# Kernel optimization log

Hardware: AMD Instinct MI355X
Metric: run time of the kernel (lower is better)

## Reference

```python
import jax, jax.numpy as jnp
import numpy as np

IMG = 256      # image size implied by 8x8 grid * scale 32
THRE = 0.5
DIS = 4        # img_dislocate_size
B = 64


def _shift_map(s, size, dis):
    # Pixel-level coordinate map for the dislocated half: cell r starts at
    # max(r*s - dis, 0) (the torch while-loop clamps negative coords to 0).
    p = jnp.arange(size)
    base = jnp.maximum((p // s) * s - dis, 0)
    return base + p % s


def _cell_norm(x, g, s):
    # Per-cell (crop) min/max normalization, matching the per-crop
    # (t - min) / (max - min + 1e-5) in HeatMaptoImg.
    b = x.shape[0]
    v = x.reshape(b, 1, g, s, g, s)
    mn = v.min(axis=(3, 5), keepdims=True)
    mx = v.max(axis=(3, 5), keepdims=True)
    return ((v - mn) / (mx - mn + 1e-5)).reshape(b, 1, g * s, g * s)


def setup_inputs() -> dict:
    key = jax.random.key(0)
    ks = jax.random.split(key, 7)
    B2 = 2 * B
    return {
        "img": jax.random.uniform(ks[0], (B, 1, IMG, IMG), jnp.float32),
        "heat8": jax.random.uniform(ks[1], (B2, 1, 8, 8), jnp.float32),
        "heat16": jax.random.uniform(ks[2], (B2, 1, 16, 16), jnp.float32),
        "heat32": jax.random.uniform(ks[3], (B2, 1, 32, 32), jnp.float32),
        "seg8": jax.random.uniform(ks[4], (B2, 1, IMG, IMG), jnp.float32),
        "seg16": jax.random.uniform(ks[5], (B2, 1, IMG, IMG), jnp.float32),
        "seg32": jax.random.uniform(ks[6], (B2, 1, IMG, IMG), jnp.float32),
    }


def reference(img, heat8, heat16, heat32, seg8, seg16, seg32):
    Bv = img.shape[0]
    label = jnp.zeros((Bv, 1, IMG, IMG), img.dtype)
    cnt = jnp.zeros_like(label)
    crops = {}
    # fine grid (scale 8) processed first, matching the reversed loop order
    for heat, seg, g in ((heat32, seg32, 32), (heat16, seg16, 16), (heat8, seg8, 8)):
        s = IMG // g                      # crop / cell size for this scale
        mask = (heat > THRE).astype(img.dtype)          # (2B,1,g,g)
        mask_pix = jnp.repeat(jnp.repeat(mask, s, axis=2), s, axis=3)  # (2B,1,256,256)
        Y = _shift_map(s, IMG, DIS)
        # dislocated half crops come from the shifted image region
        img_d = img[:, :, Y[:, None], Y[None, :]]       # (B,1,256,256)
        both = jnp.concatenate([img, img_d], axis=0)    # (2B,1,256,256)
        crops[g] = _cell_norm(both, g, s) * mask_pix
        # UnitLabels: scatter-add per-crop labels + counts, then average
        ca = mask_pix[:Bv]
        label = label + ca * seg[:Bv]
        cnt = cnt + ca
        cd = mask_pix[Bv:]
        label = label.at[:, :, Y[:, None], Y[None, :]].add(cd * seg[Bv:])
        cnt = cnt.at[:, :, Y[:, None], Y[None, :]].add(cd)
    label = label / (cnt + 1e-10)
    return (crops[32], crops[16], crops[8], label)
```

## Files before the change

kernel.cpp:

```cpp
#include <hip/hip_runtime.h>

#define IMG   256
#define IMG2  65536
#define NB    64
#define NB2   128


#define WS_A8   0
#define WS_B8   65536
#define WS_A16  131072
#define WS_B16  147456
#define WS_A32  163840
#define WS_B32  167936

template <int S, int G>
__device__ __forceinline__ void cell_stats(
    const float* __restrict__ img, const float* __restrict__ heat,
    float2* __restrict__ ws, int idx, int half, int wsbase) {
    const int b  = idx / (G * G);
    const int rr = idx % (G * G);
    const int ci = rr / G;
    const int cj = rr % G;
    const int r0 = half ? max(ci * S - 4, 0) : ci * S;
    const int c0 = half ? max(cj * S - 4, 0) : cj * S;
    const float* __restrict__ p = img + (size_t)b * IMG2 + r0 * IMG + c0;
    float mn = 3.4e38f, mx = -3.4e38f;
    for (int r = 0; r < S; ++r) {
#pragma unroll
        for (int c = 0; c < S; c += 4) {
            const float4 q = *(const float4*)(p + r * IMG + c);
            mn = fminf(mn, fminf(fminf(q.x, q.y), fminf(q.z, q.w)));
            mx = fmaxf(mx, fmaxf(fmaxf(q.x, q.y), fmaxf(q.z, q.w)));
        }
    }
    const float h   = heat[(size_t)(b + half * NB) * (G * G) + ci * G + cj];
    const float inv = (h > 0.5f ? 1.0f : 0.0f) / (mx - mn + 1e-5f);
    ws[wsbase + idx] = make_float2(mn, inv);
}

__global__ __launch_bounds__(256) void stats_kernel(
    const float* __restrict__ img,
    const float* __restrict__ heat8,
    const float* __restrict__ heat16,
    const float* __restrict__ heat32,
    float2* __restrict__ ws) {
    const int t = blockIdx.x * 256 + threadIdx.x;
    if (t < 131072) {
        const int half = t >> 16;
        cell_stats<8, 32>(img, heat32, ws, t & 65535, half,
                          half ? WS_B8 : WS_A8);
    } else if (t < 163840) {
        const int tt = t - 131072;
        const int half = tt >> 14;
        cell_stats<16, 16>(img, heat16, ws, tt & 16383, half,
                           half ? WS_B16 : WS_A16);
    } else {
        const int tt = t - 163840;
        const int half = tt >> 12;
        cell_stats<32, 8>(img, heat8, ws, tt & 4095, half,
                          half ? WS_B32 : WS_A32);
    }
}

__device__ __forceinline__ float4 nrm(float4 q, float2 st) {
    float4 o;
    o.x = (q.x - st.x) * st.y; o.y = (q.y - st.x) * st.y;
    o.z = (q.z - st.x) * st.y; o.w = (q.w - st.x) * st.y;
    return o;
}

__global__ __launch_bounds__(256) void crops_stream_kernel(
    const float* __restrict__ img,
    const float2* __restrict__ ws,
    float* __restrict__ out) {
    const int w    = threadIdx.x >> 6;
    const int lane = threadIdx.x & 63;
    const int lid  = blockIdx.x * 4 + w;
    const int b    = lid >> 8;
    const int u    = lid & 255;
    const int v0   = lane << 2;
    const int vm   = max(v0 - 4, 0);

    const float* __restrict__ ip = img + (size_t)b * IMG2;

    const int u8  = ((u >> 3) ? (u & ~7)  - 4 : 0) + (u & 7);
    const int u16 = ((u >> 4) ? (u & ~15) - 4 : 0) + (u & 15);
    const int u32 = ((u >> 5) ? (u & ~31) - 4 : 0) + (u & 31);

    const float4 xa  = *(const float4*)(ip + u   * IMG + v0);
    const float4 q08 = *(const float4*)(ip + u8  * IMG + v0);
    const float4 qm8 = *(const float4*)(ip + u8  * IMG + vm);
    const float4 q16 = *(const float4*)(ip + u16 * IMG + v0);
    const float4 qm6 = *(const float4*)(ip + u16 * IMG + vm);
    const float4 q32 = *(const float4*)(ip + u32 * IMG + v0);
    const float4 qm2 = *(const float4*)(ip + u32 * IMG + vm);

    const float2 a8  = ws[WS_A8  + ((b << 5) + (u >> 3)) * 32 + (v0 >> 3)];
    const float2 b8  = ws[WS_B8  + ((b << 5) + (u >> 3)) * 32 + (v0 >> 3)];
    const float2 a16 = ws[WS_A16 + ((b << 4) + (u >> 4)) * 16 + (v0 >> 4)];
    const float2 b16 = ws[WS_B16 + ((b << 4) + (u >> 4)) * 16 + (v0 >> 4)];
    const float2 a32 = ws[WS_A32 + ((b << 3) + (u >> 5)) *  8 + (v0 >> 5)];
    const float2 b32 = ws[WS_B32 + ((b << 3) + (u >> 5)) *  8 + (v0 >> 5)];

    const float4 s8v = (v0 < 8)  ? q08 : qm8;
    const float4 s16v = (v0 < 16) ? q16 : qm6;
    const float4 s32v = (v0 < 32) ? q32 : qm2;

    const size_t rowA = (size_t)b * IMG2 + u * IMG + v0;
    const size_t rowB = (size_t)(b + NB) * IMG2 + u * IMG + v0;
    float* __restrict__ c32 = out;
    float* __restrict__ c16 = out + (size_t)NB2 * IMG2;
    float* __restrict__ c8  = out + (size_t)2 * NB2 * IMG2;

    *(float4*)(c32 + rowA) = nrm(xa,  a8);
    *(float4*)(c32 + rowB) = nrm(s8v, b8);
    *(float4*)(c16 + rowA) = nrm(xa,  a16);
    *(float4*)(c16 + rowB) = nrm(s16v, b16);
    *(float4*)(c8  + rowA) = nrm(xa,  a32);
    *(float4*)(c8  + rowB) = nrm(s32v, b32);
}

__device__ __forceinline__ void label_rows(
    const float* __restrict__ heat8,
    const float* __restrict__ heat16,
    const float* __restrict__ heat32,
    const float* __restrict__ seg8,
    const float* __restrict__ seg16,
    const float* __restrict__ seg32,
    float* __restrict__ out,
    int b, int u0) {
    const int wave = threadIdx.x >> 6;
    const int lane = threadIdx.x & 63;
    const int u    = u0 + wave;
    const int v0   = lane << 2;
    const int vs   = min(v0 + 4, 252);

    float nu[4] = {0.f, 0.f, 0.f, 0.f};
    float de[4] = {0.f, 0.f, 0.f, 0.f};

    if (u0 >= 32 && u0 <= 248) {
        const int i1 = u + 4;
#define SCALE_F(heat, seg, g, l, s)                                           \
        {                                                                     \
            const float* __restrict__ h1 = heat + b * (g * g);                \
            const float* __restrict__ h2 = heat + (NB + b) * (g * g);         \
            const float* __restrict__ r1 = seg + (size_t)b * IMG2 + u * IMG;  \
            const float* __restrict__ r2 =                                    \
                seg + (size_t)(NB + b) * IMG2 + i1 * IMG;                     \
            const float4 sd  = *(const float4*)(r1 + v0);                     \
            const float4 sg0 = *(const float4*)(r2 + v0);                     \
            const float4 sg1 = *(const float4*)(r2 + vs);                     \
            const float hd  = h1[(u >> l) * g + (v0 >> l)];                   \
            const float hg0 = h2[(i1 >> l) * g + (v0 >> l)];                  \
            const float hg1 = h2[(i1 >> l) * g + (vs >> l)];                  \
            const float md = (hd > 0.5f) ? 1.0f : 0.0f;                       \
            const float g0 = (hg0 > 0.5f) ? 1.0f : 0.0f;                      \
            const float g1 = (hg1 > 0.5f) ? 1.0f : 0.0f;                      \
            _Pragma("unroll")                                                 \
            for (int c = 0; c < 4; ++c) {                                     \
                const int v = v0 + c;                                         \
                const float m0 = (v < (s)) ? g0 : 0.0f;                       \
                const float m1 = (v >= (s) - 4 && v <= 251) ? g1 : 0.0f;      \
                float x = ((const float*)&sd)[c] * md;                        \
                x = fmaf(m0, ((const float*)&sg0)[c], x);                     \
                x = fmaf(m1, ((const float*)&sg1)[c], x);                     \
                nu[c] += x;                                                   \
                de[c] += md + m0 + m1;                                        \
            }                                                                 \
        }
        SCALE_F(heat32, seg32, 32, 3, 8)
        SCALE_F(heat16, seg16, 16, 4, 16)
        SCALE_F(heat8,  seg8,  8,  5, 32)
#undef SCALE_F
    } else {
        const int i0  = u;
        const int i1c = min(u + 4, 255);
#define SCALE_G(heat, seg, g, l, s)                                           \
        {                                                                     \
            const float* __restrict__ h1 = heat + b * (g * g);                \
            const float* __restrict__ h2 = heat + (NB + b) * (g * g);         \
            const float* __restrict__ r1 = seg + (size_t)b * IMG2 + u * IMG;  \
            const float* __restrict__ ra =                                    \
                seg + (size_t)(NB + b) * IMG2 + i0 * IMG;                     \
            const float* __restrict__ rb =                                    \
                seg + (size_t)(NB + b) * IMG2 + i1c * IMG;                    \
            const float4 sd  = *(const float4*)(r1 + v0);                     \
            const float4 a0q = *(const float4*)(ra + v0);                     \
            const float4 a1q = *(const float4*)(ra + vs);                     \
            const float4 b0q = *(const float4*)(rb + v0);                     \
            const float4 b1q = *(const float4*)(rb + vs);                     \
            const float hd  = h1[(u >> l) * g + (v0 >> l)];                   \
            const float hA0 = h2[(i0 >> l) * g + (v0 >> l)];                  \
            const float hA1 = h2[(i0 >> l) * g + (vs >> l)];                  \
            const float hB0 = h2[(i1c >> l) * g + (v0 >> l)];                 \
            const float hB1 = h2[(i1c >> l) * g + (vs >> l)];                 \
            const float miA = (u < (s)) ? 1.0f : 0.0f;                        \
            const float miB = (u >= (s) - 4 && u <= 251) ? 1.0f : 0.0f;       \
            const float md  = (hd > 0.5f) ? 1.0f : 0.0f;                      \
            const float gA0 = miA * ((hA0 > 0.5f) ? 1.0f : 0.0f);             \
            const float gA1 = miA * ((hA1 > 0.5f) ? 1.0f : 0.0f);             \
            const float gB0 = miB * ((hB0 > 0.5f) ? 1.0f : 0.0f);             \
            const float gB1 = miB * ((hB1 > 0.5f) ? 1.0f : 0.0f);             \
            _Pragma("unroll")                                                 \
            for (int c = 0; c < 4; ++c) {                                     \
                const int v = v0 + c;                                         \
                const float mj0 = (v < (s)) ? 1.0f : 0.0f;                    \
                const float mj1 = (v >= (s) - 4 && v <= 251) ? 1.0f : 0.0f;   \
                const float w00 = gA0 * mj0, w01 = gA1 * mj1;                 \
                const float w10 = gB0 * mj0, w11 = gB1 * mj1;                 \
                float x = ((const float*)&sd)[c] * md;                        \
                x = fmaf(w00, ((const float*)&a0q)[c], x);                    \
                x = fmaf(w01, ((const float*)&a1q)[c], x);                    \
                x = fmaf(w10, ((const float*)&b0q)[c], x);                    \
                x = fmaf(w11, ((const float*)&b1q)[c], x);                    \
                nu[c] += x;                                                   \
                de[c] += md + w00 + w01 + w10 + w11;                          \
            }                                                                 \
        }
        SCALE_G(heat32, seg32, 32, 3, 8)
        SCALE_G(heat16, seg16, 16, 4, 16)
        SCALE_G(heat8,  seg8,  8,  5, 32)
#undef SCALE_G
    }

    float4 o;
    o.x = nu[0] / (de[0] + 1e-10f);
    o.y = nu[1] / (de[1] + 1e-10f);
    o.z = nu[2] / (de[2] + 1e-10f);
    o.w = nu[3] / (de[3] + 1e-10f);
    *(float4*)(out + (size_t)b * IMG2 + u * IMG + v0) = o;
}

__global__ __launch_bounds__(256) void label_kernel(
    const float* __restrict__ heat8,
    const float* __restrict__ heat16,
    const float* __restrict__ heat32,
    const float* __restrict__ seg8,
    const float* __restrict__ seg16,
    const float* __restrict__ seg32,
    float* __restrict__ out) {
    float* label = out + (size_t)3 * NB2 * IMG2;
    const int t  = blockIdx.x;
    label_rows(heat8, heat16, heat32, seg8, seg16, seg32, label,
               t >> 6, (t & 63) << 2);
}

extern "C" void kernel_launch(void* const* d_in, const int* in_sizes, int n_in,
                              void* d_out, int out_size, void* d_ws, size_t ws_size,
                              hipStream_t stream) {
    const float* img    = (const float*)d_in[0];
    const float* heat8  = (const float*)d_in[1];
    const float* heat16 = (const float*)d_in[2];
    const float* heat32 = (const float*)d_in[3];
    const float* seg8   = (const float*)d_in[4];
    const float* seg16  = (const float*)d_in[5];
    const float* seg32  = (const float*)d_in[6];

    stats_kernel<<<dim3(672), 256, 0, stream>>>(
        img, heat8, heat16, heat32, (float2*)d_ws);
    crops_stream_kernel<<<dim3(4096), 256, 0, stream>>>(
        img, (const float2*)d_ws, (float*)d_out);
    label_kernel<<<dim3(4096), 256, 0, stream>>>(
        heat8, heat16, heat32, seg8, seg16, seg32, (float*)d_out);
}
```

Measured before the change: 250.3 us.

## Build cell min/max hierarchically from 4x4 block stats and split crop writes by phase

Adds a pass computing min/max of every 4x4 pixel block, then derives each cell's min/max for all three scales (including the shifted half, which aligns to 4-pixel boundaries) by combining those block stats instead of rescanning the image per cell. The crops kernel is split into six phases across a 6x larger grid, so each thread does one load and one store rather than seven loads and six stores. This removes redundant image reads in the stats stage and cuts per-thread register pressure, at the cost of an extra kernel launch and a workspace round trip.

```diff
diff --git a/kernel.cpp b/kernel.cpp
--- a/kernel.cpp
+++ b/kernel.cpp
@@ -4,7 +4,6 @@
 #define IMG2  65536
 #define NB    64
 #define NB2   128
-
 
 #define WS_A8   0
 #define WS_B8   65536
@@ -12,112 +11,147 @@
 #define WS_B16  147456
 #define WS_A32  163840
 #define WS_B32  167936
-
-template <int S, int G>
-__device__ __forceinline__ void cell_stats(
-    const float* __restrict__ img, const float* __restrict__ heat,
-    float2* __restrict__ ws, int idx, int half, int wsbase) {
-    const int b  = idx / (G * G);
-    const int rr = idx % (G * G);
-    const int ci = rr / G;
-    const int cj = rr % G;
-    const int r0 = half ? max(ci * S - 4, 0) : ci * S;
-    const int c0 = half ? max(cj * S - 4, 0) : cj * S;
-    const float* __restrict__ p = img + (size_t)b * IMG2 + r0 * IMG + c0;
+#define WS_BLK  172032
+
+__global__ __launch_bounds__(256) void blk_kernel(
+    const float* __restrict__ img, float2* __restrict__ ws) {
+    const int wid  = blockIdx.x * 4 + (threadIdx.x >> 6);
+    const int lane = threadIdx.x & 63;
+    const int b    = wid >> 6;
+    const int r4   = wid & 63;
+    const float* __restrict__ p =
+        img + (size_t)b * IMG2 + (r4 * 4) * IMG + lane * 4;
+    const float4 q0 = *(const float4*)(p);
+    const float4 q1 = *(const float4*)(p + IMG);
+    const float4 q2 = *(const float4*)(p + 2 * IMG);
+    const float4 q3 = *(const float4*)(p + 3 * IMG);
+    const float mn01 = fminf(fminf(fminf(q0.x, q0.y), fminf(q0.z, q0.w)),
+                             fminf(fminf(q1.x, q1.y), fminf(q1.z, q1.w)));
+    const float mn23 = fminf(fminf(fminf(q2.x, q2.y), fminf(q2.z, q2.w)),
+                             fminf(fminf(q3.x, q3.y), fminf(q3.z, q3.w)));
+    const float mx01 = fmaxf(fmaxf(fmaxf(q0.x, q0.y), fmaxf(q0.z, q0.w)),
+                             fmaxf(fmaxf(q1.x, q1.y), fmaxf(q1.z, q1.w)));
+    const float mx23 = fmaxf(fmaxf(fmaxf(q2.x, q2.y), fmaxf(q2.z, q2.w)),
+                             fmaxf(fmaxf(q3.x, q3.y), fmaxf(q3.z, q3.w)));
+    ws[WS_BLK + (b << 12) + (r4 << 6) + lane] =
+        make_float2(fminf(mn01, mn23), fmaxf(mx01, mx23));
+}
+
+template <int SH>
+__device__ __forceinline__ float2 combine_blk(
+    const float2* __restrict__ blk, int b, int p0, int q0) {
     float mn = 3.4e38f, mx = -3.4e38f;
-    for (int r = 0; r < S; ++r) {
+    for (int i = 0; i < SH; ++i) {
 #pragma unroll
-        for (int c = 0; c < S; c += 4) {
-            const float4 q = *(const float4*)(p + r * IMG + c);
-            mn = fminf(mn, fminf(fminf(q.x, q.y), fminf(q.z, q.w)));
-            mx = fmaxf(mx, fmaxf(fmaxf(q.x, q.y), fmaxf(q.z, q.w)));
+        for (int j = 0; j < SH; ++j) {
+            const float2 v = blk[(b << 12) + ((p0 + i) << 6) + (q0 + j)];
+            mn = fminf(mn, v.x);
+            mx = fmaxf(mx, v.y);
         }
     }
-    const float h   = heat[(size_t)(b + half * NB) * (G * G) + ci * G + cj];
-    const float inv = (h > 0.5f ? 1.0f : 0.0f) / (mx - mn + 1e-5f);
-    ws[wsbase + idx] = make_float2(mn, inv);
-}
-
-__global__ __launch_bounds__(256) void stats_kernel(
-    const float* __restrict__ img,
+    return make_float2(mn, mx);
+}
+
+__device__ __forceinline__ float2 finish(float2 c, float h) {
+    return make_float2(c.x, (h > 0.5f ? 1.0f : 0.0f) / (c.y - c.x + 1e-5f));
+}
+
+__global__ __launch_bounds__(256) void cells_kernel(
     const float* __restrict__ heat8,
     const float* __restrict__ heat16,
     const float* __restrict__ heat32,
     float2* __restrict__ ws) {
+    const float2* __restrict__ blk = ws + WS_BLK;
     const int t = blockIdx.x * 256 + threadIdx.x;
     if (t < 131072) {
+        const int idx = t & 65535;
         const int half = t >> 16;
-        cell_stats<8, 32>(img, heat32, ws, t & 65535, half,
-                          half ? WS_B8 : WS_A8);
+        const int b = idx >> 10, ci = (idx >> 5) & 31, cj = idx & 31;
+        const int p0 = half ? max(2 * ci - 1, 0) : 2 * ci;
+        const int q0 = half ? max(2 * cj - 1, 0) : 2 * cj;
+        const float2 c = combine_blk<2>(blk, b, p0, q0);
+        const float h = heat32[(size_t)(b + half * NB) * 1024 + ci * 32 + cj];
+        ws[(half ? WS_B8 : WS_A8) + idx] = finish(c, h);
     } else if (t < 163840) {
         const int tt = t - 131072;
+        const int idx = tt & 16383;
         const int half = tt >> 14;
-        cell_stats<16, 16>(img, heat16, ws, tt & 16383, half,
-                           half ? WS_B16 : WS_A16);
+        const int b = idx >> 8, ci = (idx >> 4) & 15, cj = idx & 15;
+        const int p0 = half ? max(4 * ci - 1, 0) : 4 * ci;
+        const int q0 = half ? max(4 * cj - 1, 0) : 4 * cj;
+        const float2 c = combine_blk<4>(blk, b, p0, q0);
+        const float h = heat16[(size_t)(b + half * NB) * 256 + ci * 16 + cj];
+        ws[(half ? WS_B16 : WS_A16) + idx] = finish(c, h);
     } else {
         const int tt = t - 163840;
+        const int idx = tt & 4095;
         const int half = tt >> 12;
-        cell_stats<32, 8>(img, heat8, ws, tt & 4095, half,
-                          half ? WS_B32 : WS_A32);
+        const int b = idx >> 6, ci = (idx >> 3) & 7, cj = idx & 7;
+        const int p0 = half ? max(8 * ci - 1, 0) : 8 * ci;
+        const int q0 = half ? max(8 * cj - 1, 0) : 8 * cj;
+        const float2 c = combine_blk<8>(blk, b, p0, q0);
+        const float h = heat8[(size_t)(b + half * NB) * 64 + ci * 8 + cj];
+        ws[(half ? WS_B32 : WS_A32) + idx] = finish(c, h);
     }
-}
-
-__device__ __forceinline__ float4 nrm(float4 q, float2 st) {
-    float4 o;
-    o.x = (q.x - st.x) * st.y; o.y = (q.y - st.x) * st.y;
-    o.z = (q.z - st.x) * st.y; o.w = (q.w - st.x) * st.y;
-    return o;
 }
 
 __global__ __launch_bounds__(256) void crops_stream_kernel(
     const float* __restrict__ img,
     const float2* __restrict__ ws,
     float* __restrict__ out) {
-    const int w    = threadIdx.x >> 6;
-    const int lane = threadIdx.x & 63;
-    const int lid  = blockIdx.x * 4 + w;
-    const int b    = lid >> 8;
-    const int u    = lid & 255;
-    const int v0   = lane << 2;
-    const int vm   = max(v0 - 4, 0);
+    const int phase = blockIdx.x >> 12;
+    const int lid = (blockIdx.x & 4095) * 4 + (threadIdx.x >> 6);
+    const int b = lid >> 8, u = lid & 255;
+    const int lane = threadIdx.x & 63, v0 = lane << 2;
 
     const float* __restrict__ ip = img + (size_t)b * IMG2;
-
-    const int u8  = ((u >> 3) ? (u & ~7)  - 4 : 0) + (u & 7);
-    const int u16 = ((u >> 4) ? (u & ~15) - 4 : 0) + (u & 15);
-    const int u32 = ((u >> 5) ? (u & ~31) - 4 : 0) + (u & 31);
-
-    const float4 xa  = *(const float4*)(ip + u   * IMG + v0);
-    const float4 q08 = *(const float4*)(ip + u8  * IMG + v0);
-    const float4 qm8 = *(const float4*)(ip + u8  * IMG + vm);
-    const float4 q16 = *(const float4*)(ip + u16 * IMG + v0);
-    const float4 qm6 = *(const float4*)(ip + u16 * IMG + vm);
-    const float4 q32 = *(const float4*)(ip + u32 * IMG + v0);
-    const float4 qm2 = *(const float4*)(ip + u32 * IMG + vm);
-
-    const float2 a8  = ws[WS_A8  + ((b << 5) + (u >> 3)) * 32 + (v0 >> 3)];
-    const float2 b8  = ws[WS_B8  + ((b << 5) + (u >> 3)) * 32 + (v0 >> 3)];
-    const float2 a16 = ws[WS_A16 + ((b << 4) + (u >> 4)) * 16 + (v0 >> 4)];
-    const float2 b16 = ws[WS_B16 + ((b << 4) + (u >> 4)) * 16 + (v0 >> 4)];
-    const float2 a32 = ws[WS_A32 + ((b << 3) + (u >> 5)) *  8 + (v0 >> 5)];
-    const float2 b32 = ws[WS_B32 + ((b << 3) + (u >> 5)) *  8 + (v0 >> 5)];
-
-    const float4 s8v = (v0 < 8)  ? q08 : qm8;
-    const float4 s16v = (v0 < 16) ? q16 : qm6;
-    const float4 s32v = (v0 < 32) ? q32 : qm2;
-
-    const size_t rowA = (size_t)b * IMG2 + u * IMG + v0;
-    const size_t rowB = (size_t)(b + NB) * IMG2 + u * IMG + v0;
     float* __restrict__ c32 = out;
     float* __restrict__ c16 = out + (size_t)NB2 * IMG2;
     float* __restrict__ c8  = out + (size_t)2 * NB2 * IMG2;
 
-    *(float4*)(c32 + rowA) = nrm(xa,  a8);
-    *(float4*)(c32 + rowB) = nrm(s8v, b8);
-    *(float4*)(c16 + rowA) = nrm(xa,  a16);
-    *(float4*)(c16 + rowB) = nrm(s16v, b16);
-    *(float4*)(c8  + rowA) = nrm(xa,  a32);
-    *(float4*)(c8  + rowB) = nrm(s32v, b32);
+    int srow, scol;
+    float2 st;
+    float* optr;
+    switch (phase) {
+    case 0:
+        srow = u; scol = v0;
+        st = ws[WS_A8 + (b << 10) + ((u >> 3) << 5) + (v0 >> 3)];
+        optr = c32 + (size_t)b * IMG2;
+        break;
+    case 1:
+        srow = ((u >> 3) ? (u & ~7) - 4 : 0) + (u & 7);
+        scol = (v0 < 8) ? v0 : v0 - 4;
+        st = ws[WS_B8 + (b << 10) + ((u >> 3) << 5) + (v0 >> 3)];
+        optr = c32 + (size_t)(b + NB) * IMG2;
+        break;
+    case 2:
+        srow = u; scol = v0;
+        st = ws[WS_A16 + (b << 8) + ((u >> 4) << 4) + (v0 >> 4)];
+        optr = c16 + (size_t)b * IMG2;
+        break;
+    case 3:
+        srow = ((u >> 4) ? (u & ~15) - 4 : 0) + (u & 15);
+        scol = (v0 < 16) ? v0 : v0 - 4;
+        st = ws[WS_B16 + (b << 8) + ((u >> 4) << 4) + (v0 >> 4)];
+        optr = c16 + (size_t)(b + NB) * IMG2;
+        break;
+    case 4:
+        srow = u; scol = v0;
+        st = ws[WS_A32 + (b << 6) + ((u >> 5) << 3) + (v0 >> 5)];
+        optr = c8 + (size_t)b * IMG2;
+        break;
+    default:
+        srow = ((u >> 5) ? (u & ~31) - 4 : 0) + (u & 31);
+        scol = (v0 < 32) ? v0 : v0 - 4;
+        st = ws[WS_B32 + (b << 6) + ((u >> 5) << 3) + (v0 >> 5)];
+        optr = c8 + (size_t)(b + NB) * IMG2;
+        break;
+    }
+    const float4 q = *(const float4*)(ip + srow * IMG + scol);
+    float4 o;
+    o.x = (q.x - st.x) * st.y; o.y = (q.y - st.x) * st.y;
+    o.z = (q.z - st.x) * st.y; o.w = (q.w - st.x) * st.y;
+    *(float4*)(optr + u * IMG + v0) = o;
 }
 
 __device__ __forceinline__ void label_rows(
@@ -255,11 +289,12 @@
     const float* seg8   = (const float*)d_in[4];
     const float* seg16  = (const float*)d_in[5];
     const float* seg32  = (const float*)d_in[6];
-
-    stats_kernel<<<dim3(672), 256, 0, stream>>>(
-        img, heat8, heat16, heat32, (float2*)d_ws);
-    crops_stream_kernel<<<dim3(4096), 256, 0, stream>>>(
-        img, (const float2*)d_ws, (float*)d_out);
+    float2* ws = (float2*)d_ws;
+
+    blk_kernel<<<dim3(1024), 256, 0, stream>>>(img, ws);
+    cells_kernel<<<dim3(672), 256, 0, stream>>>(heat8, heat16, heat32, ws);
+    crops_stream_kernel<<<dim3(24576), 256, 0, stream>>>(
+        img, (const float2*)ws, (float*)d_out);
     label_kernel<<<dim3(4096), 256, 0, stream>>>(
         heat8, heat16, heat32, seg8, seg16, seg32, (float*)d_out);
 }
```

New measurement: 231.9 us. 7.3% less time.
